# Performance work log

Hardware: AMD Instinct MI355X
Metric: run time of the kernel (lower is better)

The kernel has to match this reference:

```python
import jax, jax.numpy as jnp
import numpy as np

N = 50000   # nodes
E = 800000  # edges
D = 128     # input_dim == hidden_dim
R = 8       # num_relations
B = 2       # num_blocks


def setup_inputs() -> dict:
    key = jax.random.key(0)
    ks = jax.random.split(key, 9)
    x = jax.random.normal(ks[0], (N, D), dtype=jnp.float32)
    edge_index = jax.random.randint(ks[1], (2, E), 0, N, dtype=jnp.int32)
    edge_type = jax.random.randint(ks[2], (E,), 0, R, dtype=jnp.int32)
    s_blk = 1.0 / np.sqrt(D // B)
    s_root = 1.0 / np.sqrt(D)
    W1 = jax.random.normal(ks[3], (R, B, D // B, D // B), dtype=jnp.float32) * s_blk
    root1 = jax.random.normal(ks[4], (D, D), dtype=jnp.float32) * s_root
    b1 = jnp.zeros((D,), dtype=jnp.float32)
    W2 = jax.random.normal(ks[5], (R, B, D // B, D // B), dtype=jnp.float32) * s_blk
    root2 = jax.random.normal(ks[6], (D, D), dtype=jnp.float32) * s_root
    b2 = jnp.zeros((D,), dtype=jnp.float32)
    return {"x": x, "edge_index": edge_index, "edge_type": edge_type,
            "W1": W1, "root1": root1, "b1": b1,
            "W2": W2, "root2": root2, "b2": b2}


def rgcn_conv(x, src, dst, etype, W, root, bias):
    # PyG RGCNConv (num_blocks mode): per-relation MEAN aggregation of source
    # features, block-diagonal transform, summed over relations, plus root + bias.
    # Transform is linear, so aggregate first (saves per-edge matmuls).
    n = x.shape[0]
    r, b, ib, ob = W.shape
    xs = x[src]                                   # [E, d_in] gather
    seg = dst * r + etype                          # fused (node, relation) id
    sums = jax.ops.segment_sum(xs, seg, num_segments=n * r)        # [n*r, d_in]
    cnt = jax.ops.segment_sum(jnp.ones((xs.shape[0],), xs.dtype), seg,
                              num_segments=n * r)                   # [n*r]
    mean = sums / jnp.maximum(cnt, 1.0)[:, None]   # zero where no edges
    agg = mean.reshape(n, r, b, ib)                # [n, R, blocks, in/blocks]
    out = jnp.einsum('nrbc,rbcd->nbd', agg, W).reshape(n, b * ob)
    return out + x @ root + bias


def reference(x, edge_index, edge_type, W1, root1, b1, W2, root2, b2):
    src, dst = edge_index[0], edge_index[1]
    h = jax.nn.relu(rgcn_conv(x, src, dst, edge_type, W1, root1, b1))
    # dropout(p=0.2) is identity in eval mode (reference uses eval semantics)
    return rgcn_conv(h, src, dst, edge_type, W2, root2, b2)
```

## Files before the change

### kernel.cpp

```cpp
#include <hip/hip_runtime.h>

#define NN 50000
#define EE 800000
#define DD 128
#define RR 8
#define CELLS (NN * RR)
#define TILE_N 64
#define NBLK ((NN + TILE_N - 1) / TILE_N)
#define SCAN_CHUNK 1024
#define SCAN_BLOCKS ((CELLS + SCAN_CHUNK - 1) / SCAN_CHUNK)

typedef __attribute__((ext_vector_type(4))) float f32x4;
typedef __attribute__((ext_vector_type(8))) short s16x8;
union ABu { uint4 q; s16x8 v; };


__device__ __forceinline__ unsigned int packbf2(float a, float b) {
    unsigned int ua = __float_as_uint(a);
    unsigned int ub = __float_as_uint(b);
    ua = (ua + 0x7fffu + ((ua >> 16) & 1u)) >> 16;
    ub = (ub + 0x7fffu + ((ub >> 16) & 1u)) & 0xffff0000u;
    return ua | ub;
}

__device__ __forceinline__ void upadd(float* sA, const uint4* U) {
#pragma unroll
    for (int i = 0; i < 4; ++i) {
        unsigned int uu[4] = {U[i].x, U[i].y, U[i].z, U[i].w};
#pragma unroll
        for (int j2 = 0; j2 < 4; ++j2) {
            int w = i * 8 + j2 * 2;
            sA[w]     += __uint_as_float(uu[j2] << 16);
            sA[w + 1] += __uint_as_float(uu[j2] & 0xffff0000u);
        }
    }
}

#define NB_A ((NN * 64 + 255) / 256)
#define NB_B 128
#define NB_C 32
#define NB_D ((EE + 255) / 256)

__global__ void prep_fused(const float* __restrict__ x, unsigned int* __restrict__ xb,
                           const float* __restrict__ W1, const float* __restrict__ W2,
                           unsigned int* __restrict__ Wb1, unsigned int* __restrict__ Wb2,
                           const float* __restrict__ r1, const float* __restrict__ r2,
                           unsigned int* __restrict__ rb1, unsigned int* __restrict__ rb2,
                           const int* __restrict__ dst, const int* __restrict__ et,
                           int* __restrict__ cnt) {
    int bid = blockIdx.x, tid = threadIdx.x;
    if (bid < NB_A) {
        int i = bid * 256 + tid;
        if (i < NN * 64) {
            float2 v = ((const float2*)x)[i];
            xb[i] = packbf2(v.x, v.y);
        }
    } else if (bid < NB_A + NB_B) {
        int i = (bid - NB_A) * 256 + tid;
        int kp = i & 31, n = (i >> 5) & 63, rb = i >> 11;
        int s0 = (rb * 64 + 2 * kp) * 64 + n;
        int s1 = (rb * 64 + 2 * kp + 1) * 64 + n;
        Wb1[((rb * 64 + n) * 32) + kp] = packbf2(W1[s0], W1[s1]);
        Wb2[((rb * 64 + n) * 32) + kp] = packbf2(W2[s0], W2[s1]);
    } else if (bid < NB_A + NB_B + NB_C) {
        int i = (bid - NB_A - NB_B) * 256 + tid;
        int kp = i & 63, n = i >> 6;
        int s0 = (2 * kp) * 128 + n, s1 = (2 * kp + 1) * 128 + n;
        rb1[n * 64 + kp] = packbf2(r1[s0], r1[s1]);
        rb2[n * 64 + kp] = packbf2(r2[s0], r2[s1]);
    } else {
        int e = (bid - NB_A - NB_B - NB_C) * 256 + tid;
        if (e < EE) atomicAdd(&cnt[dst[e] * RR + et[e]], 1);
    }
}


__global__ __launch_bounds__(256) void scan1(const int* __restrict__ cnt,
                                             int* __restrict__ off, int* __restrict__ bsum) {
    __shared__ int s[256];
    int tid = threadIdx.x;
    int base = blockIdx.x * SCAN_CHUNK + tid * 4;
    int v[4];
#pragma unroll
    for (int i = 0; i < 4; ++i) v[i] = (base + i < CELLS) ? cnt[base + i] : 0;
    int tot = v[0] + v[1] + v[2] + v[3];
    s[tid] = tot;
    __syncthreads();
    for (int d = 1; d < 256; d <<= 1) {
        int t = (tid >= d) ? s[tid - d] : 0;
        __syncthreads();
        s[tid] += t;
        __syncthreads();
    }
    int excl = s[tid] - tot;
    if (tid == 255) bsum[blockIdx.x] = s[255];
    int run = excl;
#pragma unroll
    for (int i = 0; i < 4; ++i) {
        if (base + i < CELLS) off[base + i] = run;
        run += v[i];
    }
}

__global__ __launch_bounds__(512) void scan2(int* __restrict__ bsum) {
    __shared__ int s[512];
    int tid = threadIdx.x;
    int v = (tid < SCAN_BLOCKS) ? bsum[tid] : 0;
    s[tid] = v;
    __syncthreads();
    for (int d = 1; d < 512; d <<= 1) {
        int t = (tid >= d) ? s[tid - d] : 0;
        __syncthreads();
        s[tid] += t;
        __syncthreads();
    }
    if (tid < SCAN_BLOCKS) bsum[tid] = s[tid] - v;
}

__global__ __launch_bounds__(256) void scan3(int* __restrict__ off, const int* __restrict__ bsum,
                                             int* __restrict__ cur) {
    int base = blockIdx.x * SCAN_CHUNK + threadIdx.x * 4;
    int add = bsum[blockIdx.x];
#pragma unroll
    for (int i = 0; i < 4; ++i) {
        int c = base + i;
        if (c < CELLS) {
            int o = off[c] + add;
            off[c] = o;
            cur[c] = o;
        }
    }
    if (blockIdx.x == 0 && threadIdx.x == 0) off[CELLS] = EE;
}

__global__ void cell_scatter(const int* __restrict__ src, const int* __restrict__ dst,
                             const int* __restrict__ et, int* __restrict__ cur,
                             int* __restrict__ esrc) {
    int e = blockIdx.x * blockDim.x + threadIdx.x;
    if (e < EE) {
        int cell = dst[e] * RR + et[e];
        int pos = atomicAdd(&cur[cell], 1);
        esrc[pos] = src[e];
    }
}

template <int RELU, int WRITEF, int WRITEB>
__global__ __launch_bounds__(256, 4) void layer_fused(
    const unsigned int* __restrict__ xgb, const int* __restrict__ esrc,
    const int* __restrict__ off,
    const unsigned int* __restrict__ Wb, const unsigned int* __restrict__ rootb,
    const float* __restrict__ bias, float* __restrict__ outf,
    unsigned int* __restrict__ outb) {

    __shared__ unsigned int SH[10240];

    int tid = threadIdx.x;
    int n0 = blockIdx.x * TILE_N;
    int e = tid & 63, q = tid >> 6;
    int w = tid >> 6, l = tid & 63;
    int quad = l >> 4, li = l & 15;
    int b = w >> 1;

    f32x4 acc[4][2];
#pragma unroll
    for (int s = 0; s < 2; ++s) {
        float bv = bias[32 * w + 16 * s + li];
#pragma unroll
        for (int mt = 0; mt < 4; ++mt) {
            acc[mt][s][0] = bv; acc[mt][s][1] = bv; acc[mt][s][2] = bv; acc[mt][s][3] = bv;
        }
    }

    int node = n0 + e;

    for (int r = 0; r < RR; ++r) {
        float sA[32];
#pragma unroll
        for (int i = 0; i < 32; ++i) sA[i] = 0.f;
        int ne = 0;
        if (node < NN) {
            int cell = node * RR + r;
            int o = off[cell];
            ne = off[cell + 1] - o;
            int t2 = 0;
            for (; t2 + 2 <= ne; t2 += 2) {
                int s0 = esrc[o + t2], s1 = esrc[o + t2 + 1];
                const uint4* p0 = (const uint4*)(xgb + (size_t)s0 * 64 + q * 16);
                const uint4* p1 = (const uint4*)(xgb + (size_t)s1 * 64 + q * 16);
                uint4 U0[4] = {p0[0], p0[1], p0[2], p0[3]};
                uint4 U1[4] = {p1[0], p1[1], p1[2], p1[3]};
                upadd(sA, U0);
                upadd(sA, U1);
            }
            if (t2 < ne) {
                int s0 = esrc[o + t2];
                const uint4* p0 = (const uint4*)(xgb + (size_t)s0 * 64 + q * 16);
                uint4 U0[4] = {p0[0], p0[1], p0[2], p0[3]};
                upadd(sA, U0);
            }
        }
        float sc = 1.0f / (float)max(ne, 1);
#pragma unroll
        for (int i = 0; i < 16; ++i)
            SH[(16 * q + i) * 66 + e] = packbf2(sA[2 * i] * sc, sA[2 * i + 1] * sc);
        __syncthreads();

        const uint4* WbB = (const uint4*)(Wb + (((size_t)r * 2 + b) * 64) * 32);
        int nl0 = (w & 1) * 32 + li;
#pragma unroll
        for (int kc = 0; kc < 2; ++kc) {
            ABu bf0, bf1;
            bf0.q = WbB[nl0 * 8 + 4 * kc + quad];
            bf1.q = WbB[(nl0 + 16) * 8 + 4 * kc + quad];
#pragma unroll
            for (int mt = 0; mt < 4; ++mt) {
                ABu af;
                int base = (32 * b + 16 * kc + 4 * quad) * 66 + 16 * mt + li;
                af.q.x = SH[base]; af.q.y = SH[base + 66];
                af.q.z = SH[base + 132]; af.q.w = SH[base + 198];
                acc[mt][0] = __builtin_amdgcn_mfma_f32_16x16x32_bf16(af.v, bf0.v, acc[mt][0], 0, 0, 0);
                acc[mt][1] = __builtin_amdgcn_mfma_f32_16x16x32_bf16(af.v, bf1.v, acc[mt][1], 0, 0, 0);
            }
        }
        __syncthreads();
    }

    if (node < NN) {
        const uint4* xr = (const uint4*)(xgb + (size_t)node * 64 + q * 16);
        uint4 X[4] = {xr[0], xr[1], xr[2], xr[3]};
#pragma unroll
        for (int i = 0; i < 4; ++i) {
            SH[(16 * q + 4 * i + 0) * 66 + e] = X[i].x;
            SH[(16 * q + 4 * i + 1) * 66 + e] = X[i].y;
            SH[(16 * q + 4 * i + 2) * 66 + e] = X[i].z;
            SH[(16 * q + 4 * i + 3) * 66 + e] = X[i].w;
        }
    } else {
#pragma unroll
        for (int i = 0; i < 16; ++i) SH[(16 * q + i) * 66 + e] = 0u;
    }
    __syncthreads();

    const uint4* RbB = (const uint4*)rootb;
#pragma unroll
    for (int kc = 0; kc < 4; ++kc) {
        ABu bf0, bf1;
        bf0.q = RbB[(32 * w + li) * 16 + 4 * kc + quad];
        bf1.q = RbB[(32 * w + 16 + li) * 16 + 4 * kc + quad];
#pragma unroll
        for (int mt = 0; mt < 4; ++mt) {
            ABu af;
            int base = (16 * kc + 4 * quad) * 66 + 16 * mt + li;
            af.q.x = SH[base]; af.q.y = SH[base + 66];
            af.q.z = SH[base + 132]; af.q.w = SH[base + 198];
            acc[mt][0] = __builtin_amdgcn_mfma_f32_16x16x32_bf16(af.v, bf0.v, acc[mt][0], 0, 0, 0);
            acc[mt][1] = __builtin_amdgcn_mfma_f32_16x16x32_bf16(af.v, bf1.v, acc[mt][1], 0, 0, 0);
        }
    }
    __syncthreads();

    float* OF = (float*)SH;
#pragma unroll
    for (int mt = 0; mt < 4; ++mt)
#pragma unroll
        for (int s = 0; s < 2; ++s)
#pragma unroll
            for (int reg = 0; reg < 4; ++reg)
                OF[(16 * mt + 4 * quad + reg) * 130 + 32 * w + 16 * s + li] = acc[mt][s][reg];
    __syncthreads();

    if (WRITEB) {
        int p = tid & 63, rg = tid >> 6;
#pragma unroll 4
        for (int it = 0; it < 16; ++it) {
            int ee = it * 4 + rg, row = n0 + ee;
            if (row < NN) {
                float v0 = OF[ee * 130 + 2 * p], v1 = OF[ee * 130 + 2 * p + 1];
                if (RELU) { v0 = fmaxf(v0, 0.f); v1 = fmaxf(v1, 0.f); }
                outb[(size_t)row * 64 + p] = packbf2(v0, v1);
            }
        }
    }
    if (WRITEF) {
        int d4 = (tid & 31) * 4, rg = tid >> 5;
#pragma unroll 4
        for (int it = 0; it < 8; ++it) {
            int ee = it * 8 + rg, row = n0 + ee;
            if (row < NN) {
                float4 v = make_float4(OF[ee * 130 + d4], OF[ee * 130 + d4 + 1],
                                       OF[ee * 130 + d4 + 2], OF[ee * 130 + d4 + 3]);
                if (RELU) {
                    v.x = fmaxf(v.x, 0.f); v.y = fmaxf(v.y, 0.f);
                    v.z = fmaxf(v.z, 0.f); v.w = fmaxf(v.w, 0.f);
                }
                *(float4*)(outf + (size_t)row * DD + d4) = v;
            }
        }
    }
}


extern "C" void kernel_launch(void* const* d_in, const int* in_sizes, int n_in,
                              void* d_out, int out_size, void* d_ws, size_t ws_size,
                              hipStream_t stream) {
    const float* x     = (const float*)d_in[0];
    const int*   ei    = (const int*)d_in[1];
    const int*   src   = ei;
    const int*   dstp  = ei + EE;
    const int*   et    = (const int*)d_in[2];
    const float* W1    = (const float*)d_in[3];
    const float* root1 = (const float*)d_in[4];
    const float* b1    = (const float*)d_in[5];
    const float* W2    = (const float*)d_in[6];
    const float* root2 = (const float*)d_in[7];
    const float* b2    = (const float*)d_in[8];
    float* out = (float*)d_out;

    unsigned int* xb  = (unsigned int*)d_ws;
    unsigned int* hb  = xb + (size_t)NN * 64;
    int* cnt  = (int*)(hb + (size_t)NN * 64);
    int* off  = cnt + CELLS;
    int* cur  = off + CELLS + 1;
    int* bsum = cur + CELLS;
    int* esrc = bsum + 512;
    unsigned int* Wb1 = (unsigned int*)(esrc + EE);
    unsigned int* Wb2 = Wb1 + 32768;
    unsigned int* rb1 = Wb2 + 32768;
    unsigned int* rb2 = rb1 + 8192;

    hipMemsetAsync(cnt, 0, CELLS * sizeof(int), stream);
    prep_fused<<<NB_A + NB_B + NB_C + NB_D, 256, 0, stream>>>(
        x, xb, W1, W2, Wb1, Wb2, root1, root2, rb1, rb2, dstp, et, cnt);
    scan1<<<SCAN_BLOCKS, 256, 0, stream>>>(cnt, off, bsum);
    scan2<<<1, 512, 0, stream>>>(bsum);
    scan3<<<SCAN_BLOCKS, 256, 0, stream>>>(off, bsum, cur);
    cell_scatter<<<(EE + 255) / 256, 256, 0, stream>>>(src, dstp, et, cur, esrc);

    layer_fused<1, 0, 1><<<NBLK, 256, 0, stream>>>(xb, esrc, off, Wb1, rb1, b1,
                                                   nullptr, hb);
    layer_fused<0, 1, 0><<<NBLK, 256, 0, stream>>>(hb, esrc, off, Wb2, rb2, b2,
                                                   out, nullptr);
}
```

Baseline: 388.6 us.

## Reorder CSR cells relation-major and gather edges wave-cooperatively per node run

Cell indexing changes from node-major to relation-major, so each wave's 16 consecutive nodes for one relation form a single contiguous edge range. Each wave walks that range cooperatively, with each lane loading one 32-bit bf16 pair per edge and flushing the mean into a double-buffered shared tile at segment boundaries. This replaces the old per-thread gather, where each thread loaded 64-byte chunks of a row and rows had very uneven edge counts. The scan2 kernel is folded into scan3 through a per-block reduction of earlier block sums, the x conversion is widened to float4, and one barrier per relation is dropped thanks to the double buffer. In exchange, the gather loop now carries shuffle-based segment-boundary logic that adds serial work.

```diff
diff --git a/kernel.cpp b/kernel.cpp
--- a/kernel.cpp
+++ b/kernel.cpp
@@ -23,20 +23,7 @@
     return ua | ub;
 }
 
-__device__ __forceinline__ void upadd(float* sA, const uint4* U) {
-#pragma unroll
-    for (int i = 0; i < 4; ++i) {
-        unsigned int uu[4] = {U[i].x, U[i].y, U[i].z, U[i].w};
-#pragma unroll
-        for (int j2 = 0; j2 < 4; ++j2) {
-            int w = i * 8 + j2 * 2;
-            sA[w]     += __uint_as_float(uu[j2] << 16);
-            sA[w + 1] += __uint_as_float(uu[j2] & 0xffff0000u);
-        }
-    }
-}
-
-#define NB_A ((NN * 64 + 255) / 256)
+#define NB_A ((NN * 32 + 255) / 256)
 #define NB_B 128
 #define NB_C 32
 #define NB_D ((EE + 255) / 256)
@@ -51,9 +38,9 @@
     int bid = blockIdx.x, tid = threadIdx.x;
     if (bid < NB_A) {
         int i = bid * 256 + tid;
-        if (i < NN * 64) {
-            float2 v = ((const float2*)x)[i];
-            xb[i] = packbf2(v.x, v.y);
+        if (i < NN * 32) {
+            float4 v = ((const float4*)x)[i];
+            ((uint2*)xb)[i] = make_uint2(packbf2(v.x, v.y), packbf2(v.z, v.w));
         }
     } else if (bid < NB_A + NB_B) {
         int i = (bid - NB_A) * 256 + tid;
@@ -70,7 +57,7 @@
         rb2[n * 64 + kp] = packbf2(r2[s0], r2[s1]);
     } else {
         int e = (bid - NB_A - NB_B - NB_C) * 256 + tid;
-        if (e < EE) atomicAdd(&cnt[dst[e] * RR + et[e]], 1);
+        if (e < EE) atomicAdd(&cnt[et[e] * NN + dst[e]], 1);
     }
 }
 
@@ -102,25 +89,21 @@
     }
 }
 
-__global__ __launch_bounds__(512) void scan2(int* __restrict__ bsum) {
-    __shared__ int s[512];
-    int tid = threadIdx.x;
-    int v = (tid < SCAN_BLOCKS) ? bsum[tid] : 0;
-    s[tid] = v;
-    __syncthreads();
-    for (int d = 1; d < 512; d <<= 1) {
-        int t = (tid >= d) ? s[tid - d] : 0;
-        __syncthreads();
-        s[tid] += t;
-        __syncthreads();
-    }
-    if (tid < SCAN_BLOCKS) bsum[tid] = s[tid] - v;
-}
-
 __global__ __launch_bounds__(256) void scan3(int* __restrict__ off, const int* __restrict__ bsum,
                                              int* __restrict__ cur) {
-    int base = blockIdx.x * SCAN_CHUNK + threadIdx.x * 4;
-    int add = bsum[blockIdx.x];
+    __shared__ int red[256];
+    int tid = threadIdx.x, bid = blockIdx.x;
+    int a = 0;
+    for (int i = tid; i < bid; i += 256) a += bsum[i];
+    red[tid] = a;
+    __syncthreads();
+#pragma unroll
+    for (int d = 128; d > 0; d >>= 1) {
+        if (tid < d) red[tid] += red[tid + d];
+        __syncthreads();
+    }
+    int add = red[0];
+    int base = bid * SCAN_CHUNK + tid * 4;
 #pragma unroll
     for (int i = 0; i < 4; ++i) {
         int c = base + i;
@@ -130,7 +113,7 @@
             cur[c] = o;
         }
     }
-    if (blockIdx.x == 0 && threadIdx.x == 0) off[CELLS] = EE;
+    if (bid == 0 && tid == 0) off[CELLS] = EE;
 }
 
 __global__ void cell_scatter(const int* __restrict__ src, const int* __restrict__ dst,
@@ -138,7 +121,7 @@
                              int* __restrict__ esrc) {
     int e = blockIdx.x * blockDim.x + threadIdx.x;
     if (e < EE) {
-        int cell = dst[e] * RR + et[e];
+        int cell = et[e] * NN + dst[e];
         int pos = atomicAdd(&cur[cell], 1);
         esrc[pos] = src[e];
     }
@@ -152,57 +135,73 @@
     const float* __restrict__ bias, float* __restrict__ outf,
     unsigned int* __restrict__ outb) {
 
-    __shared__ unsigned int SH[10240];
+    __shared__ unsigned int SH[8448];
 
     int tid = threadIdx.x;
     int n0 = blockIdx.x * TILE_N;
-    int e = tid & 63, q = tid >> 6;
     int w = tid >> 6, l = tid & 63;
     int quad = l >> 4, li = l & 15;
     int b = w >> 1;
+    int n0w = n0 + 16 * w;
+    int mtw = l * 66 + 16 * w;
 
     f32x4 acc[4][2];
 #pragma unroll
     for (int s = 0; s < 2; ++s) {
-        float bv = bias[32 * w + 16 * s + li];
+        float bb = bias[32 * w + 16 * s + li];
 #pragma unroll
         for (int mt = 0; mt < 4; ++mt) {
-            acc[mt][s][0] = bv; acc[mt][s][1] = bv; acc[mt][s][2] = bv; acc[mt][s][3] = bv;
-        }
-    }
-
-    int node = n0 + e;
+            acc[mt][s][0] = bb; acc[mt][s][1] = bb; acc[mt][s][2] = bb; acc[mt][s][3] = bb;
+        }
+    }
+
+    int bvals = 0;
+    if (l <= 16) {
+        int nd = n0w + l; if (nd > NN) nd = NN;
+        bvals = off[nd];
+    }
 
     for (int r = 0; r < RR; ++r) {
-        float sA[32];
-#pragma unroll
-        for (int i = 0; i < 32; ++i) sA[i] = 0.f;
-        int ne = 0;
-        if (node < NN) {
-            int cell = node * RR + r;
-            int o = off[cell];
-            ne = off[cell + 1] - o;
-            int t2 = 0;
-            for (; t2 + 2 <= ne; t2 += 2) {
-                int s0 = esrc[o + t2], s1 = esrc[o + t2 + 1];
-                const uint4* p0 = (const uint4*)(xgb + (size_t)s0 * 64 + q * 16);
-                const uint4* p1 = (const uint4*)(xgb + (size_t)s1 * 64 + q * 16);
-                uint4 U0[4] = {p0[0], p0[1], p0[2], p0[3]};
-                uint4 U1[4] = {p1[0], p1[1], p1[2], p1[3]};
-                upadd(sA, U0);
-                upadd(sA, U1);
-            }
-            if (t2 < ne) {
-                int s0 = esrc[o + t2];
-                const uint4* p0 = (const uint4*)(xgb + (size_t)s0 * 64 + q * 16);
-                uint4 U0[4] = {p0[0], p0[1], p0[2], p0[3]};
-                upadd(sA, U0);
-            }
-        }
-        float sc = 1.0f / (float)max(ne, 1);
-#pragma unroll
-        for (int i = 0; i < 16; ++i)
-            SH[(16 * q + i) * 66 + e] = packbf2(sA[2 * i] * sc, sA[2 * i + 1] * sc);
+        unsigned int* MT = SH + (r & 1) * 4224;
+
+        int obeg = __shfl(bvals, 0);
+        int oend = __shfl(bvals, 16);
+        int cl = 0, sbeg = obeg;
+        int nb = __shfl(bvals, 1);
+        float a0 = 0.f, a1 = 0.f;
+
+        for (int t0 = obeg; t0 < oend; t0 += 8) {
+            int m = oend - t0; if (m > 8) m = 8;
+            int sv[8]; unsigned int rv[8];
+#pragma unroll
+            for (int i = 0; i < 8; ++i) if (i < m) sv[i] = esrc[t0 + i];
+#pragma unroll
+            for (int i = 0; i < 8; ++i) if (i < m) rv[i] = xgb[(sv[i] << 6) + l];
+#pragma unroll
+            for (int i = 0; i < 8; ++i) if (i < m) {
+                int t = t0 + i;
+                while (t >= nb) {
+                    float sc = 1.0f / (float)max(nb - sbeg, 1);
+                    MT[mtw + cl] = packbf2(a0 * sc, a1 * sc);
+                    a0 = 0.f; a1 = 0.f; sbeg = nb; ++cl;
+                    nb = __shfl(bvals, min(cl + 1, 16));
+                }
+                a0 += __uint_as_float(rv[i] << 16);
+                a1 += __uint_as_float(rv[i] & 0xffff0000u);
+            }
+        }
+        while (cl < 16) {
+            float sc = 1.0f / (float)max(nb - sbeg, 1);
+            MT[mtw + cl] = packbf2(a0 * sc, a1 * sc);
+            a0 = 0.f; a1 = 0.f; sbeg = nb; ++cl;
+            nb = __shfl(bvals, min(cl + 1, 16));
+        }
+
+        int bvn = 0;
+        if (l <= 16 && r + 1 < RR) {
+            int nd = n0w + l; if (nd > NN) nd = NN;
+            bvn = off[(r + 1) * NN + nd];
+        }
         __syncthreads();
 
         const uint4* WbB = (const uint4*)(Wb + (((size_t)r * 2 + b) * 64) * 32);
@@ -216,28 +215,31 @@
             for (int mt = 0; mt < 4; ++mt) {
                 ABu af;
                 int base = (32 * b + 16 * kc + 4 * quad) * 66 + 16 * mt + li;
-                af.q.x = SH[base]; af.q.y = SH[base + 66];
-                af.q.z = SH[base + 132]; af.q.w = SH[base + 198];
+                af.q.x = MT[base]; af.q.y = MT[base + 66];
+                af.q.z = MT[base + 132]; af.q.w = MT[base + 198];
                 acc[mt][0] = __builtin_amdgcn_mfma_f32_16x16x32_bf16(af.v, bf0.v, acc[mt][0], 0, 0, 0);
                 acc[mt][1] = __builtin_amdgcn_mfma_f32_16x16x32_bf16(af.v, bf1.v, acc[mt][1], 0, 0, 0);
             }
         }
-        __syncthreads();
-    }
-
-    if (node < NN) {
-        const uint4* xr = (const uint4*)(xgb + (size_t)node * 64 + q * 16);
-        uint4 X[4] = {xr[0], xr[1], xr[2], xr[3]};
-#pragma unroll
-        for (int i = 0; i < 4; ++i) {
-            SH[(16 * q + 4 * i + 0) * 66 + e] = X[i].x;
-            SH[(16 * q + 4 * i + 1) * 66 + e] = X[i].y;
-            SH[(16 * q + 4 * i + 2) * 66 + e] = X[i].z;
-            SH[(16 * q + 4 * i + 3) * 66 + e] = X[i].w;
-        }
-    } else {
-#pragma unroll
-        for (int i = 0; i < 16; ++i) SH[(16 * q + i) * 66 + e] = 0u;
+        bvals = bvn;
+    }
+
+    {
+        int node = n0 + l;
+        if (node < NN) {
+            const uint4* xr = (const uint4*)(xgb + (size_t)node * 64 + w * 16);
+            uint4 X[4] = {xr[0], xr[1], xr[2], xr[3]};
+#pragma unroll
+            for (int i = 0; i < 4; ++i) {
+                SH[(16 * w + 4 * i + 0) * 66 + l] = X[i].x;
+                SH[(16 * w + 4 * i + 1) * 66 + l] = X[i].y;
+                SH[(16 * w + 4 * i + 2) * 66 + l] = X[i].z;
+                SH[(16 * w + 4 * i + 3) * 66 + l] = X[i].w;
+            }
+        } else {
+#pragma unroll
+            for (int i = 0; i < 16; ++i) SH[(16 * w + i) * 66 + l] = 0u;
+        }
     }
     __syncthreads();
 
@@ -332,7 +334,6 @@
     prep_fused<<<NB_A + NB_B + NB_C + NB_D, 256, 0, stream>>>(
         x, xb, W1, W2, Wb1, Wb2, root1, root2, rb1, rb2, dstp, et, cnt);
     scan1<<<SCAN_BLOCKS, 256, 0, stream>>>(cnt, off, bsum);
-    scan2<<<1, 512, 0, stream>>>(bsum);
     scan3<<<SCAN_BLOCKS, 256, 0, stream>>>(off, bsum, cur);
     cell_scatter<<<(EE + 255) / 256, 256, 0, stream>>>(src, dstp, et, cur, esrc);
 
```

New measurement: 468.5 us. 20.6% more time.
